# Optimization experiments

Measured on AMD Instinct MI355X. Metric: run time of the kernel, lower is better.

Reference implementation:

```python
import jax, jax.numpy as jnp
import numpy as np


def setup_inputs() -> dict:
    key = jax.random.key(0)
    k1, k2 = jax.random.split(key)
    x1 = jax.random.normal(k1, (16, 512, 64, 64), dtype=jnp.float32)
    x2 = jax.random.normal(k2, (16, 512, 64, 64), dtype=jnp.float32)
    return {"x1": x1, "x2": x2}


def reference(x1, x2):
    B, C1, H, W = x1.shape
    C2 = x2.shape[1]
    N = H * W
    x1_d = x1.reshape(B, C1, N)  # (B, C1, N)
    x2_d = x2.reshape(B, C2, N)  # (B, C2, N)
    # energy[b, i, j] = sum_n x1_d[b, i, n] * x2_d[b, j, n]
    energy = jnp.einsum('bin,bjn->bij', x1_d, x2_d)  # (B, C1, C2)
    attention = jax.nn.softmax(energy, axis=-1)       # softmax over C2
    # attention^T @ x1_d -> (B, C2, N)
    attention_value = jnp.einsum('bij,bin->bjn', attention, x1_d).reshape(B, C2, H, W)
    out = jnp.concatenate((x1, attention_value), axis=1)  # (B, C1+C2, H, W)
    return (out, attention)
```

## Files before the change

kernel.cpp:

```cpp
#include <hip/hip_runtime.h>

typedef short bf16x8 __attribute__((ext_vector_type(8)));
typedef float f32x4  __attribute__((ext_vector_type(4)));
typedef unsigned int u32;
typedef unsigned short u16;

#define NBATCH 16
#define C      512
#define NPIX   4096
#define ATT_OFF ((size_t)NBATCH * 1024 * NPIX)

typedef __attribute__((address_space(1))) const u32* gp_t;
typedef __attribute__((address_space(3))) u32* lp_t;

__device__ __forceinline__ void splitpair(u32 u0, u32 u1, u32& h, u32& l) {
    h = __builtin_amdgcn_perm(u1, u0, 0x07060302u);
    const u32 m0 = u0 & 0xFFFF0000u, m1 = u1 & 0xFFFF0000u;
    const float l0 = __uint_as_float(u0) - __uint_as_float(m0);
    const float l1 = __uint_as_float(u1) - __uint_as_float(m1);
    l = __builtin_amdgcn_perm(__float_as_uint(l1), __float_as_uint(l0), 0x07060302u);
}

__global__ __launch_bounds__(256, 2) void gemm1_energy(
    const float* __restrict__ x1, const float* __restrict__ x2,
    float* __restrict__ out)
{
    __shared__ __align__(16) float Asm[2][128 * 32];
    __shared__ __align__(16) float Bsm[2][128 * 32];

    const int tid  = threadIdx.x;
    const int lane = tid & 63;
    const int w    = tid >> 6;
    const int wr   = (w >> 1) * 64;
    const int wc   = (w & 1) * 64;
    const int r16  = lane & 15;
    const int g    = lane >> 4;

    const int gid = (blockIdx.x & 7) * 64 + (blockIdx.x >> 3);
    const int b   = gid >> 5;
    const int ib  = ((gid >> 3) & 3) * 128;
    const int jb  = ((gid >> 1) & 3) * 128;
    const int ks  = gid & 1;
    const int ko  = ks * 2048;

    const int lrow  = lane >> 3;
    const int chunk = lane & 7;
    const float* srcA[4];
    const float* srcB[4];
    #pragma unroll
    for (int q = 0; q < 4; ++q) {
        const int row = w * 32 + q * 8 + lrow;
        const int sc  = (chunk ^ ((row >> 1) & 7)) * 4;
        srcA[q] = x1 + (size_t)(b * C + ib + row) * NPIX + ko + sc;
        srcB[q] = x2 + (size_t)(b * C + jb + row) * NPIX + ko + sc;
    }

    auto stage = [&](int kt, int buf) {
        #pragma unroll
        for (int q = 0; q < 4; ++q) {
            __builtin_amdgcn_global_load_lds((gp_t)(const void*)(srcA[q] + kt * 32),
                                             (lp_t)(void*)&Asm[buf][(w * 32 + q * 8) * 32], 16, 0, 0);
            __builtin_amdgcn_global_load_lds((gp_t)(const void*)(srcB[q] + kt * 32),
                                             (lp_t)(void*)&Bsm[buf][(w * 32 + q * 8) * 32], 16, 0, 0);
        }
    };

    const f32x4 zero4 = {0.f, 0.f, 0.f, 0.f};
    f32x4 acc[4][4];
    #pragma unroll
    for (int i = 0; i < 4; ++i)
        #pragma unroll
        for (int j = 0; j < 4; ++j) acc[i][j] = zero4;

    union B8 { bf16x8 v; u32 u[4]; };

    stage(0, 0);

    for (int kt = 0; kt < 64; ++kt) {
        const int buf = kt & 1;
        __syncthreads();

        B8 ah[4], al[4], bh[4], bl[4];
        uint4 UA[4][2], UB[4][2];
        #pragma unroll
        for (int f = 0; f < 4; ++f) {
            const int ar = wr + f * 16 + r16;
            const float* abase = &Asm[buf][ar * 32];
            UA[f][0] = *(const uint4*)(abase + (((2 * g)     ^ ((ar >> 1) & 7)) * 4));
            UA[f][1] = *(const uint4*)(abase + (((2 * g + 1) ^ ((ar >> 1) & 7)) * 4));
            const int br = wc + f * 16 + r16;
            const float* bbase = &Bsm[buf][br * 32];
            UB[f][0] = *(const uint4*)(bbase + (((2 * g)     ^ ((br >> 1) & 7)) * 4));
            UB[f][1] = *(const uint4*)(bbase + (((2 * g + 1) ^ ((br >> 1) & 7)) * 4));
        }
        if (kt < 63) stage(kt + 1, buf ^ 1);

        #pragma unroll
        for (int f = 0; f < 4; ++f) {
            splitpair(UA[f][0].x, UA[f][0].y, ah[f].u[0], al[f].u[0]);
            splitpair(UA[f][0].z, UA[f][0].w, ah[f].u[1], al[f].u[1]);
            splitpair(UA[f][1].x, UA[f][1].y, ah[f].u[2], al[f].u[2]);
            splitpair(UA[f][1].z, UA[f][1].w, ah[f].u[3], al[f].u[3]);
            splitpair(UB[f][0].x, UB[f][0].y, bh[f].u[0], bl[f].u[0]);
            splitpair(UB[f][0].z, UB[f][0].w, bh[f].u[1], bl[f].u[1]);
            splitpair(UB[f][1].x, UB[f][1].y, bh[f].u[2], bl[f].u[2]);
            splitpair(UB[f][1].z, UB[f][1].w, bh[f].u[3], bl[f].u[3]);
        }

        __builtin_amdgcn_s_setprio(1);
        #pragma unroll
        for (int fi = 0; fi < 4; ++fi)
            #pragma unroll
            for (int fj = 0; fj < 4; ++fj) {
                acc[fi][fj] = __builtin_amdgcn_mfma_f32_16x16x32_bf16(ah[fi].v, bh[fj].v, acc[fi][fj], 0, 0, 0);
                acc[fi][fj] = __builtin_amdgcn_mfma_f32_16x16x32_bf16(ah[fi].v, bl[fj].v, acc[fi][fj], 0, 0, 0);
                acc[fi][fj] = __builtin_amdgcn_mfma_f32_16x16x32_bf16(al[fi].v, bh[fj].v, acc[fi][fj], 0, 0, 0);
            }
        __builtin_amdgcn_s_setprio(0);
    }

    float* dst = (ks == 0) ? (out + ATT_OFF + (size_t)b * C * C)
                           : (out + (size_t)(b * 1024 + 512) * NPIX);
    #pragma unroll
    for (int fi = 0; fi < 4; ++fi)
        #pragma unroll
        for (int fj = 0; fj < 4; ++fj) {
            const int j = jb + wc + fj * 16 + r16;
            #pragma unroll
            for (int q = 0; q < 4; ++q) {
                const int i = ib + wr + fi * 16 + g * 4 + q;
                dst[(size_t)i * C + j] = acc[fi][fj][q];
            }
        }
}

__global__ __launch_bounds__(256) void softmax_rows(float* __restrict__ out)
{
    const int bi = blockIdx.x;
    const int b  = bi >> 9;
    const int i  = bi & 511;
    float* p        = out + ATT_OFF + (size_t)bi * C;
    const float* pk = out + (size_t)(b * 1024 + 512) * NPIX + (size_t)i * C;

    const int t = threadIdx.x;
    const int lane = t & 63, wid = t >> 6;
    __shared__ float red[8];

    float a = p[t] + pk[t];
    float c = p[t + 256] + pk[t + 256];
    float m = fmaxf(a, c);
    #pragma unroll
    for (int o = 32; o; o >>= 1) m = fmaxf(m, __shfl_xor(m, o));
    if (lane == 0) red[wid] = m;
    __syncthreads();
    m = fmaxf(fmaxf(red[0], red[1]), fmaxf(red[2], red[3]));

    float e0 = __expf(a - m), e1 = __expf(c - m);
    float s = e0 + e1;
    #pragma unroll
    for (int o = 32; o; o >>= 1) s += __shfl_xor(s, o);
    if (lane == 0) red[4 + wid] = s;
    __syncthreads();
    s = (red[4] + red[5]) + (red[6] + red[7]);
    const float inv = 1.0f / s;
    p[t]       = e0 * inv;
    p[t + 256] = e1 * inv;
}

#define KST 36

__global__ __launch_bounds__(256, 3) void gemm2_av(
    const float* __restrict__ x1, float* __restrict__ out)
{
    __shared__ __align__(16) u16 Aj[2][128 * KST];
    __shared__ __align__(16) u16 Bn[2][128 * KST];

    const float* att = out + ATT_OFF;
    const int tid  = threadIdx.x;
    const int lane = tid & 63;
    const int wid  = tid >> 6;
    const int wr   = (wid >> 1) * 64;
    const int wc   = (wid & 1) * 64;
    const int r16  = lane & 15;
    const int g    = lane >> 4;

    const int gid = (blockIdx.x & 7) * 256 + (blockIdx.x >> 3);
    const int b   = gid >> 7;
    const int jt  = (gid >> 5) & 3;
    const int nt  = gid & 31;
    const int jb  = jt * 128;
    const int nb  = nt * 128;

    const int col = (tid & 31) * 4;
    const int ksr = (tid >> 5) * 4;

    const float* ap0 = att + (size_t)b * C * C    + (size_t)ksr * C    + jb + col;
    const float* bp0 = x1  + (size_t)b * C * NPIX + (size_t)ksr * NPIX + nb + col;
    float* cpy = out + (size_t)(b * 1024 + ksr) * NPIX + nb + col;

    f32x4 La[4], Lb[4];

    auto loadk = [&](int kt) {
        #pragma unroll
        for (int i = 0; i < 4; ++i) {
            La[i] = *(const f32x4*)(ap0 + (size_t)(kt * 32 + i) * C);
            Lb[i] = *(const f32x4*)(bp0 + (size_t)(kt * 32 + i) * NPIX);
        }
    };

    auto stage = [&](int kt, int buf) {
        u32 sa[8], sb[8];
        #pragma unroll
        for (int jj = 0; jj < 4; ++jj) {
            sa[jj * 2]     = __builtin_amdgcn_perm(__float_as_uint(La[1][jj]), __float_as_uint(La[0][jj]), 0x07060302u);
            sa[jj * 2 + 1] = __builtin_amdgcn_perm(__float_as_uint(La[3][jj]), __float_as_uint(La[2][jj]), 0x07060302u);
            sb[jj * 2]     = __builtin_amdgcn_perm(__float_as_uint(Lb[1][jj]), __float_as_uint(Lb[0][jj]), 0x07060302u);
            sb[jj * 2 + 1] = __builtin_amdgcn_perm(__float_as_uint(Lb[3][jj]), __float_as_uint(Lb[2][jj]), 0x07060302u);
        }
        #pragma unroll
        for (int jj = 0; jj < 4; ++jj) {
            *(uint2*)((char*)Aj[buf] + ((col + jj) * KST + ksr) * 2) = make_uint2(sa[jj * 2], sa[jj * 2 + 1]);
            *(uint2*)((char*)Bn[buf] + ((col + jj) * KST + ksr) * 2) = make_uint2(sb[jj * 2], sb[jj * 2 + 1]);
        }
        if (jt == 0) {
            #pragma unroll
            for (int i = 0; i < 4; ++i)
                *(f32x4*)(cpy + (size_t)(kt * 32 + i) * NPIX) = Lb[i];
        }
    };

    const f32x4 zero4 = {0.f, 0.f, 0.f, 0.f};
    f32x4 acc[4][4];
    #pragma unroll
    for (int i = 0; i < 4; ++i)
        #pragma unroll
        for (int j = 0; j < 4; ++j) acc[i][j] = zero4;

    loadk(0);
    stage(0, 0);

    for (int kt = 0; kt < 16; ++kt) {
        if (kt < 15) loadk(kt + 1);
        __syncthreads();
        const int buf = kt & 1;

        union { bf16x8 v; uint2 u2[2]; } fa[4], fb[4];
        #pragma unroll
        for (int f = 0; f < 4; ++f) {
            const int aj = wr + f * 16 + r16;
            fa[f].u2[0] = *(const uint2*)(&Aj[buf][aj * KST + g * 8]);
            fa[f].u2[1] = *(const uint2*)(&Aj[buf][aj * KST + g * 8 + 4]);
            const int bn = wc + f * 16 + r16;
            fb[f].u2[0] = *(const uint2*)(&Bn[buf][bn * KST + g * 8]);
            fb[f].u2[1] = *(const uint2*)(&Bn[buf][bn * KST + g * 8 + 4]);
        }
        __builtin_amdgcn_s_setprio(1);
        #pragma unroll
        for (int fi = 0; fi < 4; ++fi)
            #pragma unroll
            for (int fj = 0; fj < 4; ++fj)
                acc[fi][fj] = __builtin_amdgcn_mfma_f32_16x16x32_bf16(fa[fi].v, fb[fj].v, acc[fi][fj], 0, 0, 0);
        __builtin_amdgcn_s_setprio(0);
        if (kt < 15) stage(kt + 1, buf ^ 1);
    }

    #pragma unroll
    for (int fi = 0; fi < 4; ++fi)
        #pragma unroll
        for (int fj = 0; fj < 4; ++fj) {
            const int n = nb + wc + fj * 16 + r16;
            #pragma unroll
            for (int q = 0; q < 4; ++q) {
                const int j = jb + wr + fi * 16 + g * 4 + q;
                out[(size_t)(b * 1024 + 512 + j) * NPIX + n] = acc[fi][fj][q];
            }
        }
}

extern "C" void kernel_launch(void* const* d_in, const int* in_sizes, int n_in,
                              void* d_out, int out_size, void* d_ws, size_t ws_size,
                              hipStream_t stream) {
    const float* x1 = (const float*)d_in[0];
    const float* x2 = (const float*)d_in[1];
    float* out = (float*)d_out;
    (void)in_sizes; (void)n_in; (void)out_size; (void)d_ws; (void)ws_size;

    gemm1_energy<<<dim3(512),  dim3(256), 0, stream>>>(x1, x2, out);
    softmax_rows<<<dim3(8192), dim3(256), 0, stream>>>(out);
    gemm2_av    <<<dim3(2048), dim3(256), 0, stream>>>(x1, out);
}
```

Baseline: 235.0 us.

## Load GEMM1 fragments directly from global into registers, drop LDS staging

```diff
diff --git a/kernel.cpp b/kernel.cpp
--- a/kernel.cpp
+++ b/kernel.cpp
@@ -4,14 +4,12 @@
 typedef float f32x4  __attribute__((ext_vector_type(4)));
 typedef unsigned int u32;
 typedef unsigned short u16;
+typedef u32 u32x4 __attribute__((ext_vector_type(4)));
 
 #define NBATCH 16
 #define C      512
 #define NPIX   4096
 #define ATT_OFF ((size_t)NBATCH * 1024 * NPIX)
-
-typedef __attribute__((address_space(1))) const u32* gp_t;
-typedef __attribute__((address_space(3))) u32* lp_t;
 
 __device__ __forceinline__ void splitpair(u32 u0, u32 u1, u32& h, u32& l) {
     h = __builtin_amdgcn_perm(u1, u0, 0x07060302u);
@@ -25,9 +23,6 @@
     const float* __restrict__ x1, const float* __restrict__ x2,
     float* __restrict__ out)
 {
-    __shared__ __align__(16) float Asm[2][128 * 32];
-    __shared__ __align__(16) float Bsm[2][128 * 32];
-
     const int tid  = threadIdx.x;
     const int lane = tid & 63;
     const int w    = tid >> 6;
@@ -37,33 +32,19 @@
     const int g    = lane >> 4;
 
     const int gid = (blockIdx.x & 7) * 64 + (blockIdx.x >> 3);
-    const int b   = gid >> 5;
-    const int ib  = ((gid >> 3) & 3) * 128;
-    const int jb  = ((gid >> 1) & 3) * 128;
-    const int ks  = gid & 1;
+    const int jb  = (gid & 3) * 128;
+    const int ib  = ((gid >> 2) & 3) * 128;
+    const int b   = (gid >> 4) & 15;
+    const int ks  = gid >> 8;
     const int ko  = ks * 2048;
 
-    const int lrow  = lane >> 3;
-    const int chunk = lane & 7;
-    const float* srcA[4];
-    const float* srcB[4];
-    #pragma unroll
-    for (int q = 0; q < 4; ++q) {
-        const int row = w * 32 + q * 8 + lrow;
-        const int sc  = (chunk ^ ((row >> 1) & 7)) * 4;
-        srcA[q] = x1 + (size_t)(b * C + ib + row) * NPIX + ko + sc;
-        srcB[q] = x2 + (size_t)(b * C + jb + row) * NPIX + ko + sc;
-    }
-
-    auto stage = [&](int kt, int buf) {
-        #pragma unroll
-        for (int q = 0; q < 4; ++q) {
-            __builtin_amdgcn_global_load_lds((gp_t)(const void*)(srcA[q] + kt * 32),
-                                             (lp_t)(void*)&Asm[buf][(w * 32 + q * 8) * 32], 16, 0, 0);
-            __builtin_amdgcn_global_load_lds((gp_t)(const void*)(srcB[q] + kt * 32),
-                                             (lp_t)(void*)&Bsm[buf][(w * 32 + q * 8) * 32], 16, 0, 0);
-        }
-    };
+    const float* Ap[4];
+    const float* Bp[4];
+    #pragma unroll
+    for (int f = 0; f < 4; ++f) {
+        Ap[f] = x1 + (size_t)(b * C + ib + wr + f * 16 + r16) * NPIX + ko + g * 8;
+        Bp[f] = x2 + (size_t)(b * C + jb + wc + f * 16 + r16) * NPIX + ko + g * 8;
+    }
 
     const f32x4 zero4 = {0.f, 0.f, 0.f, 0.f};
     f32x4 acc[4][4];
@@ -74,27 +55,17 @@
 
     union B8 { bf16x8 v; u32 u[4]; };
 
-    stage(0, 0);
+    u32x4 UA[4][2], UB[4][2];
+    #pragma unroll
+    for (int f = 0; f < 4; ++f) {
+        UA[f][0] = *(const u32x4*)(Ap[f]);
+        UA[f][1] = *(const u32x4*)(Ap[f] + 4);
+        UB[f][0] = *(const u32x4*)(Bp[f]);
+        UB[f][1] = *(const u32x4*)(Bp[f] + 4);
+    }
 
     for (int kt = 0; kt < 64; ++kt) {
-        const int buf = kt & 1;
-        __syncthreads();
-
         B8 ah[4], al[4], bh[4], bl[4];
-        uint4 UA[4][2], UB[4][2];
-        #pragma unroll
-        for (int f = 0; f < 4; ++f) {
-            const int ar = wr + f * 16 + r16;
-            const float* abase = &Asm[buf][ar * 32];
-            UA[f][0] = *(const uint4*)(abase + (((2 * g)     ^ ((ar >> 1) & 7)) * 4));
-            UA[f][1] = *(const uint4*)(abase + (((2 * g + 1) ^ ((ar >> 1) & 7)) * 4));
-            const int br = wc + f * 16 + r16;
-            const float* bbase = &Bsm[buf][br * 32];
-            UB[f][0] = *(const uint4*)(bbase + (((2 * g)     ^ ((br >> 1) & 7)) * 4));
-            UB[f][1] = *(const uint4*)(bbase + (((2 * g + 1) ^ ((br >> 1) & 7)) * 4));
-        }
-        if (kt < 63) stage(kt + 1, buf ^ 1);
-
         #pragma unroll
         for (int f = 0; f < 4; ++f) {
             splitpair(UA[f][0].x, UA[f][0].y, ah[f].u[0], al[f].u[0]);
@@ -107,6 +78,17 @@
             splitpair(UB[f][1].z, UB[f][1].w, bh[f].u[3], bl[f].u[3]);
         }
 
+        if (kt < 63) {
+            const int off = (kt + 1) * 32;
+            #pragma unroll
+            for (int f = 0; f < 4; ++f) {
+                UA[f][0] = *(const u32x4*)(Ap[f] + off);
+                UA[f][1] = *(const u32x4*)(Ap[f] + off + 4);
+                UB[f][0] = *(const u32x4*)(Bp[f] + off);
+                UB[f][1] = *(const u32x4*)(Bp[f] + off + 4);
+            }
+        }
+
         __builtin_amdgcn_s_setprio(1);
         #pragma unroll
         for (int fi = 0; fi < 4; ++fi)
@@ -185,9 +167,9 @@
     const int g    = lane >> 4;
 
     const int gid = (blockIdx.x & 7) * 256 + (blockIdx.x >> 3);
+    const int jt  = gid & 3;
+    const int nt  = (gid >> 2) & 31;
     const int b   = gid >> 7;
-    const int jt  = (gid >> 5) & 3;
-    const int nt  = gid & 31;
     const int jb  = jt * 128;
     const int nb  = nt * 128;
 
```

New measurement: 363.7 us. 54.7% more time.

## Split energy GEMM K four ways with single-buffered LDS and higher occupancy

Applied to the files above, without the earlier changes.

```diff
diff --git a/kernel.cpp b/kernel.cpp
--- a/kernel.cpp
+++ b/kernel.cpp
@@ -21,12 +21,12 @@
     l = __builtin_amdgcn_perm(__float_as_uint(l1), __float_as_uint(l0), 0x07060302u);
 }
 
-__global__ __launch_bounds__(256, 2) void gemm1_energy(
+__global__ __launch_bounds__(256, 4) void gemm1_energy(
     const float* __restrict__ x1, const float* __restrict__ x2,
     float* __restrict__ out)
 {
-    __shared__ __align__(16) float Asm[2][128 * 32];
-    __shared__ __align__(16) float Bsm[2][128 * 32];
+    __shared__ __align__(16) float Asm[128 * 32];
+    __shared__ __align__(16) float Bsm[128 * 32];
 
     const int tid  = threadIdx.x;
     const int lane = tid & 63;
@@ -36,12 +36,12 @@
     const int r16  = lane & 15;
     const int g    = lane >> 4;
 
-    const int gid = (blockIdx.x & 7) * 64 + (blockIdx.x >> 3);
-    const int b   = gid >> 5;
-    const int ib  = ((gid >> 3) & 3) * 128;
-    const int jb  = ((gid >> 1) & 3) * 128;
-    const int ks  = gid & 1;
-    const int ko  = ks * 2048;
+    const int gid = (blockIdx.x & 7) * 128 + (blockIdx.x >> 3);
+    const int jb  = (gid & 3) * 128;
+    const int ib  = ((gid >> 2) & 3) * 128;
+    const int b   = (gid >> 4) & 15;
+    const int ks  = gid >> 8;
+    const int ko  = ks * 1024;
 
     const int lrow  = lane >> 3;
     const int chunk = lane & 7;
@@ -55,13 +55,13 @@
         srcB[q] = x2 + (size_t)(b * C + jb + row) * NPIX + ko + sc;
     }
 
-    auto stage = [&](int kt, int buf) {
+    auto stage = [&](int kt) {
         #pragma unroll
         for (int q = 0; q < 4; ++q) {
             __builtin_amdgcn_global_load_lds((gp_t)(const void*)(srcA[q] + kt * 32),
-                                             (lp_t)(void*)&Asm[buf][(w * 32 + q * 8) * 32], 16, 0, 0);
+                                             (lp_t)(void*)&Asm[(w * 32 + q * 8) * 32], 16, 0, 0);
             __builtin_amdgcn_global_load_lds((gp_t)(const void*)(srcB[q] + kt * 32),
-                                             (lp_t)(void*)&Bsm[buf][(w * 32 + q * 8) * 32], 16, 0, 0);
+                                             (lp_t)(void*)&Bsm[(w * 32 + q * 8) * 32], 16, 0, 0);
         }
     };
 
@@ -74,27 +74,25 @@
 
     union B8 { bf16x8 v; u32 u[4]; };
 
-    stage(0, 0);
-
-    for (int kt = 0; kt < 64; ++kt) {
-        const int buf = kt & 1;
+    stage(0);
+
+    for (int kt = 0; kt < 32; ++kt) {
         __syncthreads();
 
-        B8 ah[4], al[4], bh[4], bl[4];
         uint4 UA[4][2], UB[4][2];
         #pragma unroll
         for (int f = 0; f < 4; ++f) {
             const int ar = wr + f * 16 + r16;
-            const float* abase = &Asm[buf][ar * 32];
+            const float* abase = &Asm[ar * 32];
             UA[f][0] = *(const uint4*)(abase + (((2 * g)     ^ ((ar >> 1) & 7)) * 4));
             UA[f][1] = *(const uint4*)(abase + (((2 * g + 1) ^ ((ar >> 1) & 7)) * 4));
             const int br = wc + f * 16 + r16;
-            const float* bbase = &Bsm[buf][br * 32];
+            const float* bbase = &Bsm[br * 32];
             UB[f][0] = *(const uint4*)(bbase + (((2 * g)     ^ ((br >> 1) & 7)) * 4));
             UB[f][1] = *(const uint4*)(bbase + (((2 * g + 1) ^ ((br >> 1) & 7)) * 4));
         }
-        if (kt < 63) stage(kt + 1, buf ^ 1);
-
+
+        B8 ah[4], al[4], bh[4], bl[4];
         #pragma unroll
         for (int f = 0; f < 4; ++f) {
             splitpair(UA[f][0].x, UA[f][0].y, ah[f].u[0], al[f].u[0]);
@@ -107,6 +105,9 @@
             splitpair(UB[f][1].z, UB[f][1].w, bh[f].u[3], bl[f].u[3]);
         }
 
+        __syncthreads();
+        if (kt + 1 < 32) stage(kt + 1);
+
         __builtin_amdgcn_s_setprio(1);
         #pragma unroll
         for (int fi = 0; fi < 4; ++fi)
@@ -119,8 +120,9 @@
         __builtin_amdgcn_s_setprio(0);
     }
 
-    float* dst = (ks == 0) ? (out + ATT_OFF + (size_t)b * C * C)
-                           : (out + (size_t)(b * 1024 + 512) * NPIX);
+    float* dst = (ks == 0)
+        ? (out + ATT_OFF + (size_t)b * C * C)
+        : (out + (size_t)(b * 1024 + 512) * NPIX + (size_t)(ks - 1) * C * C);
     #pragma unroll
     for (int fi = 0; fi < 4; ++fi)
         #pragma unroll
@@ -146,8 +148,8 @@
     const int lane = t & 63, wid = t >> 6;
     __shared__ float red[8];
 
-    float a = p[t] + pk[t];
-    float c = p[t + 256] + pk[t + 256];
+    float a = p[t]       + pk[t]                 + pk[C * C + t]       + pk[2 * C * C + t];
+    float c = p[t + 256] + pk[t + 256] + pk[C * C + t + 256] + pk[2 * C * C + t + 256];
     float m = fmaxf(a, c);
     #pragma unroll
     for (int o = 32; o; o >>= 1) m = fmaxf(m, __shfl_xor(m, o));
@@ -185,9 +187,9 @@
     const int g    = lane >> 4;
 
     const int gid = (blockIdx.x & 7) * 256 + (blockIdx.x >> 3);
+    const int jt  = gid & 3;
+    const int nt  = (gid >> 2) & 31;
     const int b   = gid >> 7;
-    const int jt  = (gid >> 5) & 3;
-    const int nt  = gid & 31;
     const int jb  = jt * 128;
     const int nb  = nt * 128;
 
@@ -285,7 +287,7 @@
     float* out = (float*)d_out;
     (void)in_sizes; (void)n_in; (void)out_size; (void)d_ws; (void)ws_size;
 
-    gemm1_energy<<<dim3(512),  dim3(256), 0, stream>>>(x1, x2, out);
+    gemm1_energy<<<dim3(1024), dim3(256), 0, stream>>>(x1, x2, out);
     softmax_rows<<<dim3(8192), dim3(256), 0, stream>>>(out);
     gemm2_av    <<<dim3(2048), dim3(256), 0, stream>>>(x1, out);
 }
```

Result: slower. 517.2 us (+120.1%).
